# Performance work log

Measured on AMD Instinct MI355X. Metric: run time of the kernel, lower is better.

## Reference

```python
import jax, jax.numpy as jnp
import numpy as np

N_NODES = 50000
NODE_DIM = 128
HIDDEN = 128
N_EDGES = 1600000
N_POSTS = 8192


def setup_inputs() -> dict:
    key = jax.random.key(0)
    ks = jax.random.split(key, 12)
    glorot = lambda k, shp: jax.random.normal(k, shp, jnp.float32) * (1.0 / np.sqrt(shp[0]))
    inp = {
        "node_features": jax.random.normal(ks[0], (N_NODES, NODE_DIM), jnp.float32),
        "edge_index": jax.random.randint(ks[1], (2, N_EDGES), 0, N_NODES, jnp.int32),
        "post_mask": jax.random.randint(ks[2], (N_POSTS,), 0, N_NODES, jnp.int32),
        # node_encoder: node_dim -> hidden
        "W_enc": glorot(ks[3], (NODE_DIM, HIDDEN)),
        "b_enc": jnp.zeros((HIDDEN,), jnp.float32),
        # conv1/conv2: hidden -> hidden
        "W1": glorot(ks[4], (HIDDEN, HIDDEN)),
        "b1": jnp.zeros((HIDDEN,), jnp.float32),
        "W2": glorot(ks[5], (HIDDEN, HIDDEN)),
        "b2": jnp.zeros((HIDDEN,), jnp.float32),
        # output head: hidden -> hidden//2 -> 1
        "W_o1": glorot(ks[6], (HIDDEN, HIDDEN // 2)),
        "b_o1": jnp.zeros((HIDDEN // 2,), jnp.float32),
        "W_o2": glorot(ks[7], (HIDDEN // 2, 1)),
        "b_o2": jnp.zeros((1,), jnp.float32),
    }
    return inp


def _aggregate(h, src, dst, n_nodes):
    # sum_{e: dst[e]=v} h[src[e]]  -- vectorized scatter-add (segment_sum)
    return jax.ops.segment_sum(h[src], dst, num_segments=n_nodes)


def reference(node_features, edge_index, post_mask,
              W_enc, b_enc, W1, b1, W2, b2, W_o1, b_o1, W_o2, b_o2):
    src, dst = edge_index[0], edge_index[1]
    n = node_features.shape[0]

    h = jax.nn.relu(node_features @ W_enc + b_enc)          # [N, H]
    agg = _aggregate(h, src, dst, n)                        # [N, H]
    h = jax.nn.relu((agg + h) @ W1 + b1)
    agg = _aggregate(h, src, dst, n)
    h = jax.nn.relu((agg + h) @ W2 + b2)

    post = h[post_mask]                                     # [P, H]
    hid = jax.nn.relu(post @ W_o1 + b_o1)                   # [P, H//2]
    logits = (hid @ W_o2 + b_o2).squeeze(-1)                # [P]
    return jax.nn.sigmoid(logits)
```

## Files before the change

kernel.cpp:

```cpp
#include <hip/hip_runtime.h>
#include <math.h>


typedef unsigned long long u64;

#define RB_SIZE    4096
#define RB_ROUNDS  16
#define BUCKET_CAP 9216

__global__ __launch_bounds__(1024) void scan_part(const int* __restrict__ in,
                                                  int* __restrict__ bsum, int n) {
    __shared__ int red[1024];
    int i = blockIdx.x * 1024 + threadIdx.x;
    red[threadIdx.x] = (i < n) ? in[i] : 0;
    __syncthreads();
    for (int d = 512; d; d >>= 1) {
        if (threadIdx.x < d) red[threadIdx.x] += red[threadIdx.x + d];
        __syncthreads();
    }
    if (threadIdx.x == 0) bsum[blockIdx.x] = red[0];
}

__global__ __launch_bounds__(256) void scan_tops_par(const int* __restrict__ bsum,
                                                     int* __restrict__ bbase, int nb) {
    __shared__ int buf[256];
    int tid = threadIdx.x;
    int v = (tid < nb) ? bsum[tid] : 0;
    buf[tid] = v;
    __syncthreads();
    for (int s = 1; s < 256; s <<= 1) {
        int u = (tid >= s) ? buf[tid - s] : 0;
        __syncthreads();
        buf[tid] += u;
        __syncthreads();
    }
    if (tid < nb) bbase[tid] = buf[tid] - v;
}

__global__ __launch_bounds__(1024) void scan_final(const int* __restrict__ in,
                                                   const int* __restrict__ bbase,
                                                   int* __restrict__ out, int n) {
    __shared__ int buf[1024];
    int tid = threadIdx.x;
    int i = blockIdx.x * 1024 + tid;
    int c = (i < n) ? in[i] : 0;
    buf[tid] = c;
    __syncthreads();
    for (int d = 1; d < 1024; d <<= 1) {
        int v = (tid >= d) ? buf[tid - d] : 0;
        __syncthreads();
        buf[tid] += v;
        __syncthreads();
    }
    if (i < n) out[i] = bbase[blockIdx.x] + buf[tid] - c;
}

__global__ __launch_bounds__(256) void radix_hist_hi(const int* __restrict__ dstArr,
                                                     int* __restrict__ blockhist,
                                                     int E, int NBLK) {
    __shared__ int cnt[256];
    cnt[threadIdx.x] = 0;
    __syncthreads();
    int base = blockIdx.x * RB_SIZE;
    for (int t = threadIdx.x; t < RB_SIZE; t += 256) {
        int i = base + t;
        if (i < E) atomicAdd(&cnt[dstArr[i] >> 8], 1);
    }
    __syncthreads();
    blockhist[threadIdx.x * NBLK + blockIdx.x] = cnt[threadIdx.x];
}

__global__ __launch_bounds__(256) void radix_scatter_hi(const int* __restrict__ dstArr,
                                                        const int* __restrict__ srcArr,
                                                        u64* __restrict__ recOut,
                                                        const int* __restrict__ blockbase,
                                                        int E, int NBLK) {
    __shared__ int cursor[256];
    __shared__ int gbase[256];
    __shared__ int cnt[256 * 4];
    __shared__ int wbase[256 * 4];
    int tid = threadIdx.x;
    int wid = tid >> 6, lane = tid & 63;
    cursor[tid] = 0;
    gbase[tid] = blockbase[tid * NBLK + blockIdx.x];
    int base = blockIdx.x * RB_SIZE;
    __syncthreads();
    for (int r = 0; r < RB_ROUNDS; ++r) {
        int i = base + r * 256 + tid;
        bool valid = (i < E);
        int d = 0;
        u64 rec = 0;
        if (valid) {
            int dv = dstArr[i];
            rec = ((u64)(unsigned)srcArr[i] << 32) | (unsigned)dv;
            d = dv >> 8;
        }
        ((int4*)cnt)[tid] = make_int4(0, 0, 0, 0);
        u64 mask = ~0ull;
#pragma unroll
        for (int b = 0; b < 8; ++b) {
            int bit = (d >> b) & 1;
            u64 bal = __ballot(bit);
            mask &= bit ? bal : ~bal;
        }
        mask &= __ballot(valid ? 1 : 0);
        int rank = __popcll(mask & (((u64)1 << lane) - 1));
        int wtot = __popcll(mask);
        __syncthreads();
        if (valid && rank == 0) cnt[d * 4 + wid] = wtot;
        __syncthreads();
        {
            int run = cursor[tid];
#pragma unroll
            for (int w = 0; w < 4; ++w) {
                wbase[tid * 4 + w] = run;
                run += cnt[tid * 4 + w];
            }
            cursor[tid] = run;
        }
        __syncthreads();
        if (valid) recOut[gbase[d] + wbase[d * 4 + wid] + rank] = rec;
        __syncthreads();
    }
}

__global__ __launch_bounds__(256) void bucket_kernel(const u64* __restrict__ rec,
                                                     const int* __restrict__ blockbase,
                                                     int* __restrict__ csr_src,
                                                     int* __restrict__ offs,
                                                     int E, int N, int NBLK, int NDIG) {
    __shared__ int srcs[BUCKET_CAP];
    __shared__ unsigned char lob[BUCKET_CAP];
    __shared__ int binb[256];
    __shared__ int cursor[256];
    __shared__ int cnt4[256 * 4];
    __shared__ int wbase4[256 * 4];
    int g = blockIdx.x;
    int tid = threadIdx.x;
    int wid = tid >> 6, lane = tid & 63;
    int gbeg = blockbase[g * NBLK];
    int gend = (g + 1 < NDIG) ? blockbase[(g + 1) * NBLK] : E;
    int cnt = gend - gbeg;
    if (cnt > BUCKET_CAP) cnt = BUCKET_CAP;
    binb[tid] = 0;
    __syncthreads();
    for (int i = tid; i < cnt; i += 256) {
        u64 r = rec[gbeg + i];
        srcs[i] = (int)(r >> 32);
        int lo = (int)(r & 255);
        lob[i] = (unsigned char)lo;
        atomicAdd(&binb[lo], 1);
    }
    __syncthreads();
    int c = binb[tid];
    cursor[tid] = c;
    __syncthreads();
    for (int s = 1; s < 256; s <<= 1) {
        int v = (tid >= s) ? cursor[tid - s] : 0;
        __syncthreads();
        cursor[tid] += v;
        __syncthreads();
    }
    int excl = cursor[tid] - c;
    __syncthreads();
    binb[tid] = excl;
    cursor[tid] = excl;
    int v = g * 256 + tid;
    if (v < N) offs[v] = gbeg + excl;
    if (g == NDIG - 1 && tid == 0) offs[N] = E;
    __syncthreads();
    int nrounds = (cnt + 255) >> 8;
    for (int r = 0; r < nrounds; ++r) {
        int i = r * 256 + tid;
        bool valid = (i < cnt);
        int d = valid ? (int)lob[i] : 0;
        ((int4*)cnt4)[tid] = make_int4(0, 0, 0, 0);
        u64 mask = ~0ull;
#pragma unroll
        for (int b = 0; b < 8; ++b) {
            int bit = (d >> b) & 1;
            u64 bal = __ballot(bit);
            mask &= bit ? bal : ~bal;
        }
        mask &= __ballot(valid ? 1 : 0);
        int rank = __popcll(mask & (((u64)1 << lane) - 1));
        int wtot = __popcll(mask);
        __syncthreads();
        if (valid && rank == 0) cnt4[d * 4 + wid] = wtot;
        __syncthreads();
        {
            int run = cursor[tid];
#pragma unroll
            for (int w = 0; w < 4; ++w) {
                wbase4[tid * 4 + w] = run;
                run += cnt4[tid * 4 + w];
            }
            cursor[tid] = run;
        }
        __syncthreads();
        if (valid) csr_src[gbeg + wbase4[d * 4 + wid] + rank] = srcs[i];
        __syncthreads();
    }
}

template <bool FUSE>
__global__ __launch_bounds__(256) void gemm128(const float* __restrict__ A,
                                               const float* __restrict__ A2,
                                               const float* __restrict__ W,
                                               const float* __restrict__ bias,
                                               float* __restrict__ out, int M) {
    __shared__ float As[128 * 64];
    __shared__ float Ws[64 * 128];
    int tid = threadIdx.x;
    int tx = tid & 15;
    int ty = tid >> 4;
    int row0 = blockIdx.x * 128;

    float acc[8][8];
#pragma unroll
    for (int r = 0; r < 8; ++r)
#pragma unroll
        for (int c = 0; c < 8; ++c) acc[r][c] = 0.f;

    const float4* A4 = (const float4*)A;
    const float4* A24 = (const float4*)A2;
    const float4* W4 = (const float4*)W;
    float4* As4 = (float4*)As;
    float4* Ws4 = (float4*)Ws;
    int swz = ty & 7;

    for (int kh = 0; kh < 2; ++kh) {
        __syncthreads();
#pragma unroll
        for (int j = 0; j < 8; ++j) {
            int idx = tid + 256 * j;
            int r = idx >> 4, kf = idx & 15;
            int gr = row0 + r;
            float4 v = make_float4(0.f, 0.f, 0.f, 0.f);
            if (gr < M) {
                v = A4[gr * 32 + kh * 16 + kf];
                if (FUSE) {
                    float4 u = A24[gr * 32 + kh * 16 + kf];
                    v.x += u.x; v.y += u.y; v.z += u.z; v.w += u.w;
                }
            }
            As4[r * 16 + (kf ^ ((r >> 3) & 7))] = v;
            int k = idx >> 5, cf = idx & 31;
            Ws4[k * 32 + cf] = W4[(kh * 64 + k) * 32 + cf];
        }
        __syncthreads();

#pragma unroll 2
        for (int k4 = 0; k4 < 16; ++k4) {
            float4 a[8];
#pragma unroll
            for (int r = 0; r < 8; ++r)
                a[r] = As4[(ty * 8 + r) * 16 + (k4 ^ swz)];
#pragma unroll
            for (int kk = 0; kk < 4; ++kk) {
                float4 b0 = Ws4[(k4 * 4 + kk) * 32 + tx];
                float4 b1 = Ws4[(k4 * 4 + kk) * 32 + 16 + tx];
#pragma unroll
                for (int r = 0; r < 8; ++r) {
                    float av = (kk == 0) ? a[r].x : (kk == 1) ? a[r].y
                             : (kk == 2) ? a[r].z : a[r].w;
                    acc[r][0] = fmaf(av, b0.x, acc[r][0]);
                    acc[r][1] = fmaf(av, b0.y, acc[r][1]);
                    acc[r][2] = fmaf(av, b0.z, acc[r][2]);
                    acc[r][3] = fmaf(av, b0.w, acc[r][3]);
                    acc[r][4] = fmaf(av, b1.x, acc[r][4]);
                    acc[r][5] = fmaf(av, b1.y, acc[r][5]);
                    acc[r][6] = fmaf(av, b1.z, acc[r][6]);
                    acc[r][7] = fmaf(av, b1.w, acc[r][7]);
                }
            }
        }
    }

    float4 bv0 = ((const float4*)bias)[tx];
    float4 bv1 = ((const float4*)bias)[16 + tx];
    float4* out4 = (float4*)out;
#pragma unroll
    for (int r = 0; r < 8; ++r) {
        int gr = row0 + ty * 8 + r;
        if (gr < M) {
            float4 o0, o1;
            o0.x = fmaxf(acc[r][0] + bv0.x, 0.f);
            o0.y = fmaxf(acc[r][1] + bv0.y, 0.f);
            o0.z = fmaxf(acc[r][2] + bv0.z, 0.f);
            o0.w = fmaxf(acc[r][3] + bv0.w, 0.f);
            o1.x = fmaxf(acc[r][4] + bv1.x, 0.f);
            o1.y = fmaxf(acc[r][5] + bv1.y, 0.f);
            o1.z = fmaxf(acc[r][6] + bv1.z, 0.f);
            o1.w = fmaxf(acc[r][7] + bv1.w, 0.f);
            out4[gr * 32 + tx] = o0;
            out4[gr * 32 + 16 + tx] = o1;
        }
    }
}

__global__ __launch_bounds__(256) void aggregate_kernel(const float* __restrict__ h,
                                                        const int* __restrict__ offs,
                                                        const int* __restrict__ csr_src,
                                                        float* __restrict__ agg, int n) {
    int w = (blockIdx.x * 256 + threadIdx.x) >> 6;
    int lane = threadIdx.x & 63;
    int half = lane >> 5;
    int l32 = lane & 31;
    int node = w * 2 + half;
    bool nvalid = node < n;
    int beg = 0, deg = 0;
    if (nvalid) {
        beg = offs[node];
        deg = offs[node + 1] - beg;
    }
    int mdeg = max(deg, __shfl_xor(deg, 32));
    const float4* h4 = (const float4*)h;
    float ax = 0.f, ay = 0.f, az = 0.f, aw = 0.f;
    for (int base = 0; base < mdeg; base += 32) {
        int idx = base + l32;
        int sv = (nvalid && idx < deg) ? csr_src[beg + idx] : 0;
        int nk = mdeg - base; if (nk > 32) nk = 32;
#pragma unroll 4
        for (int j = 0; j < nk; ++j) {
            int s = __shfl(sv, (half << 5) | j);
            if (base + j < deg) {
                float4 r = h4[s * 32 + l32];
                ax += r.x; ay += r.y; az += r.z; aw += r.w;
            }
        }
    }
    if (nvalid) {
        float4 o = make_float4(ax, ay, az, aw);
        ((float4*)agg)[(size_t)node * 32 + l32] = o;
    }
}

__global__ __launch_bounds__(256) void head_kernel(const float* __restrict__ h,
                                                   const int* __restrict__ mask,
                                                   const float* __restrict__ Wo1,
                                                   const float* __restrict__ bo1,
                                                   const float* __restrict__ Wo2,
                                                   const float* __restrict__ bo2,
                                                   float* __restrict__ out, int P) {
    __shared__ float hids[4][64];
    int wid = threadIdx.x >> 6;
    int lane = threadIdx.x & 63;
    int p = blockIdx.x * 4 + wid;
    if (p >= P) return;
    int node = mask[p];
    const float* row = h + (size_t)node * 128;
    float acc = 0.f;
#pragma unroll 4
    for (int k = 0; k < 128; ++k)
        acc = fmaf(row[k], Wo1[k * 64 + lane], acc);
    hids[wid][lane] = fmaxf(acc + bo1[lane], 0.f);
    if (lane == 0) {
        double lg = 0.0;
        for (int j = 0; j < 64; ++j)
            lg = fma((double)hids[wid][j], (double)Wo2[j], lg);
        lg += (double)bo2[0];
        out[p] = (float)(1.0 / (1.0 + exp(-lg)));
    }
}

extern "C" void kernel_launch(void* const* d_in, const int* in_sizes, int n_in,
                              void* d_out, int out_size, void* d_ws, size_t ws_size,
                              hipStream_t stream) {
    const float* NF   = (const float*)d_in[0];
    const int*   EI   = (const int*)d_in[1];
    const int*   MASK = (const int*)d_in[2];
    const float* Wenc = (const float*)d_in[3];
    const float* benc = (const float*)d_in[4];
    const float* W1   = (const float*)d_in[5];
    const float* b1   = (const float*)d_in[6];
    const float* W2   = (const float*)d_in[7];
    const float* b2   = (const float*)d_in[8];
    const float* Wo1  = (const float*)d_in[9];
    const float* bo1  = (const float*)d_in[10];
    const float* Wo2  = (const float*)d_in[11];
    const float* bo2  = (const float*)d_in[12];
    float* out = (float*)d_out;

    const int N = in_sizes[0] / 128;
    const int E = in_sizes[1] / 2;
    const int P = in_sizes[2];

    char* ws = (char*)d_ws;
    size_t off = 0;
    auto alloc = [&](size_t bytes) {
        char* pp = ws + off;
        off += (bytes + 255) & ~(size_t)255;
        return pp;
    };
    float* h       = (float*)alloc((size_t)N * 128 * 4);
    float* agg     = (float*)alloc((size_t)N * 128 * 4);
    int*   offs    = (int*)alloc((size_t)(N + 1) * 4);
    int*   csr_src = (int*)alloc((size_t)E * 4);
    const int NBLK = (E + RB_SIZE - 1) / RB_SIZE;
    int*   bh      = (int*)alloc((size_t)256 * NBLK * 4);
    int*   bb      = (int*)alloc((size_t)256 * NBLK * 4);
    int*   bsum    = (int*)alloc(256 * 4);
    int*   bbase   = (int*)alloc(256 * 4);
    u64* rec_a = (u64*)h;

    const int* src = EI;
    const int* dst = EI + E;

    const int NDIG = (N + 255) >> 8;
    const int L = NDIG * NBLK;
    const int nscanL = (L + 1023) / 1024;

    radix_hist_hi<<<NBLK, 256, 0, stream>>>(dst, bh, E, NBLK);
    scan_part<<<nscanL, 1024, 0, stream>>>(bh, bsum, L);
    scan_tops_par<<<1, 256, 0, stream>>>(bsum, bbase, nscanL);
    scan_final<<<nscanL, 1024, 0, stream>>>(bh, bbase, bb, L);
    radix_scatter_hi<<<NBLK, 256, 0, stream>>>(dst, src, rec_a, bb, E, NBLK);

    bucket_kernel<<<NDIG, 256, 0, stream>>>(rec_a, bb, csr_src, offs, E, N, NBLK, NDIG);

    int gblocks = (N + 127) / 128;
    int ablocks = ((N + 1) / 2 + 3) / 4;
    gemm128<false><<<gblocks, 256, 0, stream>>>(NF, nullptr, Wenc, benc, h, N);
    aggregate_kernel<<<ablocks, 256, 0, stream>>>(h, offs, csr_src, agg, N);
    gemm128<true><<<gblocks, 256, 0, stream>>>(h, agg, W1, b1, h, N);
    aggregate_kernel<<<ablocks, 256, 0, stream>>>(h, offs, csr_src, agg, N);
    gemm128<true><<<gblocks, 256, 0, stream>>>(h, agg, W2, b2, h, N);
    head_kernel<<<(P + 3) / 4, 256, 0, stream>>>(h, MASK, Wo1, bo1, Wo2, bo2, out, P);
}
```

Baseline: 395.6 us.

## Fuse radix-sort CSR build into one cooperative kernel with grid syncs

Merges the histogram, three scan kernels, the scatter and the bucket sort into a single cooperative kernel separated by grid.sync barriers, with a per-digit scan over blocks replacing the flat global scan. The aim is to cut five kernel launches and their gaps, and to shrink the block-histogram buffer to NDIG rows. In exchange, the grid (about 391 blocks with 56KB LDS each) must be co-resident or the cooperative launch fails, and the large shared allocation lowers occupancy for every phase.

```diff
diff --git a/kernel.cpp b/kernel.cpp
--- a/kernel.cpp
+++ b/kernel.cpp
@@ -1,5 +1,8 @@
 #include <hip/hip_runtime.h>
+#include <hip/hip_cooperative_groups.h>
 #include <math.h>
+
+namespace cg = cooperative_groups;
 
 
 typedef unsigned long long u64;
@@ -8,198 +11,186 @@
 #define RB_ROUNDS  16
 #define BUCKET_CAP 9216
 
-__global__ __launch_bounds__(1024) void scan_part(const int* __restrict__ in,
-                                                  int* __restrict__ bsum, int n) {
-    __shared__ int red[1024];
-    int i = blockIdx.x * 1024 + threadIdx.x;
-    red[threadIdx.x] = (i < n) ? in[i] : 0;
-    __syncthreads();
-    for (int d = 512; d; d >>= 1) {
-        if (threadIdx.x < d) red[threadIdx.x] += red[threadIdx.x + d];
-        __syncthreads();
-    }
-    if (threadIdx.x == 0) bsum[blockIdx.x] = red[0];
-}
-
-__global__ __launch_bounds__(256) void scan_tops_par(const int* __restrict__ bsum,
-                                                     int* __restrict__ bbase, int nb) {
-    __shared__ int buf[256];
+__global__ __launch_bounds__(256) void sort_coop(const int* __restrict__ dstArr,
+                                                 const int* __restrict__ srcArr,
+                                                 u64* __restrict__ rec,
+                                                 int* __restrict__ bh,
+                                                 int* __restrict__ dtot,
+                                                 int* __restrict__ csr_src,
+                                                 int* __restrict__ offs,
+                                                 int E, int N, int NBLK, int NDIG) {
+    __shared__ int smem[14080];
+    int* srcs = smem;
+    unsigned char* lob = (unsigned char*)(smem + 9216);
+    int* A = smem + 11520;
+    int* B = smem + 11776;
+    int* C = smem + 12032;
+    int* D = smem + 13056;
+
+    cg::grid_group grid = cg::this_grid();
     int tid = threadIdx.x;
-    int v = (tid < nb) ? bsum[tid] : 0;
-    buf[tid] = v;
-    __syncthreads();
-    for (int s = 1; s < 256; s <<= 1) {
-        int u = (tid >= s) ? buf[tid - s] : 0;
-        __syncthreads();
-        buf[tid] += u;
-        __syncthreads();
-    }
-    if (tid < nb) bbase[tid] = buf[tid] - v;
-}
-
-__global__ __launch_bounds__(1024) void scan_final(const int* __restrict__ in,
-                                                   const int* __restrict__ bbase,
-                                                   int* __restrict__ out, int n) {
-    __shared__ int buf[1024];
-    int tid = threadIdx.x;
-    int i = blockIdx.x * 1024 + tid;
-    int c = (i < n) ? in[i] : 0;
-    buf[tid] = c;
-    __syncthreads();
-    for (int d = 1; d < 1024; d <<= 1) {
-        int v = (tid >= d) ? buf[tid - d] : 0;
-        __syncthreads();
-        buf[tid] += v;
-        __syncthreads();
-    }
-    if (i < n) out[i] = bbase[blockIdx.x] + buf[tid] - c;
-}
-
-__global__ __launch_bounds__(256) void radix_hist_hi(const int* __restrict__ dstArr,
-                                                     int* __restrict__ blockhist,
-                                                     int E, int NBLK) {
-    __shared__ int cnt[256];
-    cnt[threadIdx.x] = 0;
-    __syncthreads();
-    int base = blockIdx.x * RB_SIZE;
-    for (int t = threadIdx.x; t < RB_SIZE; t += 256) {
-        int i = base + t;
-        if (i < E) atomicAdd(&cnt[dstArr[i] >> 8], 1);
-    }
-    __syncthreads();
-    blockhist[threadIdx.x * NBLK + blockIdx.x] = cnt[threadIdx.x];
-}
-
-__global__ __launch_bounds__(256) void radix_scatter_hi(const int* __restrict__ dstArr,
-                                                        const int* __restrict__ srcArr,
-                                                        u64* __restrict__ recOut,
-                                                        const int* __restrict__ blockbase,
-                                                        int E, int NBLK) {
-    __shared__ int cursor[256];
-    __shared__ int gbase[256];
-    __shared__ int cnt[256 * 4];
-    __shared__ int wbase[256 * 4];
-    int tid = threadIdx.x;
+    int b = blockIdx.x;
     int wid = tid >> 6, lane = tid & 63;
-    cursor[tid] = 0;
-    gbase[tid] = blockbase[tid * NBLK + blockIdx.x];
-    int base = blockIdx.x * RB_SIZE;
-    __syncthreads();
-    for (int r = 0; r < RB_ROUNDS; ++r) {
-        int i = base + r * 256 + tid;
-        bool valid = (i < E);
-        int d = 0;
-        u64 rec = 0;
-        if (valid) {
-            int dv = dstArr[i];
-            rec = ((u64)(unsigned)srcArr[i] << 32) | (unsigned)dv;
-            d = dv >> 8;
-        }
-        ((int4*)cnt)[tid] = make_int4(0, 0, 0, 0);
-        u64 mask = ~0ull;
-#pragma unroll
-        for (int b = 0; b < 8; ++b) {
-            int bit = (d >> b) & 1;
-            u64 bal = __ballot(bit);
-            mask &= bit ? bal : ~bal;
-        }
-        mask &= __ballot(valid ? 1 : 0);
-        int rank = __popcll(mask & (((u64)1 << lane) - 1));
-        int wtot = __popcll(mask);
-        __syncthreads();
-        if (valid && rank == 0) cnt[d * 4 + wid] = wtot;
-        __syncthreads();
-        {
-            int run = cursor[tid];
-#pragma unroll
-            for (int w = 0; w < 4; ++w) {
-                wbase[tid * 4 + w] = run;
-                run += cnt[tid * 4 + w];
-            }
-            cursor[tid] = run;
-        }
-        __syncthreads();
-        if (valid) recOut[gbase[d] + wbase[d * 4 + wid] + rank] = rec;
-        __syncthreads();
-    }
-}
-
-__global__ __launch_bounds__(256) void bucket_kernel(const u64* __restrict__ rec,
-                                                     const int* __restrict__ blockbase,
-                                                     int* __restrict__ csr_src,
-                                                     int* __restrict__ offs,
-                                                     int E, int N, int NBLK, int NDIG) {
-    __shared__ int srcs[BUCKET_CAP];
-    __shared__ unsigned char lob[BUCKET_CAP];
-    __shared__ int binb[256];
-    __shared__ int cursor[256];
-    __shared__ int cnt4[256 * 4];
-    __shared__ int wbase4[256 * 4];
-    int g = blockIdx.x;
-    int tid = threadIdx.x;
-    int wid = tid >> 6, lane = tid & 63;
-    int gbeg = blockbase[g * NBLK];
-    int gend = (g + 1 < NDIG) ? blockbase[(g + 1) * NBLK] : E;
-    int cnt = gend - gbeg;
-    if (cnt > BUCKET_CAP) cnt = BUCKET_CAP;
-    binb[tid] = 0;
-    __syncthreads();
-    for (int i = tid; i < cnt; i += 256) {
-        u64 r = rec[gbeg + i];
-        srcs[i] = (int)(r >> 32);
-        int lo = (int)(r & 255);
-        lob[i] = (unsigned char)lo;
-        atomicAdd(&binb[lo], 1);
-    }
-    __syncthreads();
-    int c = binb[tid];
-    cursor[tid] = c;
-    __syncthreads();
-    for (int s = 1; s < 256; s <<= 1) {
-        int v = (tid >= s) ? cursor[tid - s] : 0;
-        __syncthreads();
-        cursor[tid] += v;
-        __syncthreads();
-    }
-    int excl = cursor[tid] - c;
-    __syncthreads();
-    binb[tid] = excl;
-    cursor[tid] = excl;
-    int v = g * 256 + tid;
-    if (v < N) offs[v] = gbeg + excl;
-    if (g == NDIG - 1 && tid == 0) offs[N] = E;
-    __syncthreads();
-    int nrounds = (cnt + 255) >> 8;
-    for (int r = 0; r < nrounds; ++r) {
-        int i = r * 256 + tid;
-        bool valid = (i < cnt);
-        int d = valid ? (int)lob[i] : 0;
-        ((int4*)cnt4)[tid] = make_int4(0, 0, 0, 0);
-        u64 mask = ~0ull;
-#pragma unroll
-        for (int b = 0; b < 8; ++b) {
-            int bit = (d >> b) & 1;
-            u64 bal = __ballot(bit);
-            mask &= bit ? bal : ~bal;
-        }
-        mask &= __ballot(valid ? 1 : 0);
-        int rank = __popcll(mask & (((u64)1 << lane) - 1));
-        int wtot = __popcll(mask);
-        __syncthreads();
-        if (valid && rank == 0) cnt4[d * 4 + wid] = wtot;
-        __syncthreads();
-        {
-            int run = cursor[tid];
-#pragma unroll
-            for (int w = 0; w < 4; ++w) {
-                wbase4[tid * 4 + w] = run;
-                run += cnt4[tid * 4 + w];
-            }
-            cursor[tid] = run;
-        }
-        __syncthreads();
-        if (valid) csr_src[gbeg + wbase4[d * 4 + wid] + rank] = srcs[i];
-        __syncthreads();
+
+    if (b < NBLK) {
+        A[tid] = 0;
+        __syncthreads();
+        int base = b * RB_SIZE;
+        for (int t = tid; t < RB_SIZE; t += 256) {
+            int i = base + t;
+            if (i < E) atomicAdd(&A[dstArr[i] >> 8], 1);
+        }
+        __syncthreads();
+        if (tid < NDIG) bh[tid * NBLK + b] = A[tid];
+    }
+    grid.sync();
+
+    if (b < NDIG) {
+        int running = 0;
+        for (int base = 0; base < NBLK; base += 512) {
+            int i0 = base + tid, i1 = base + tid + 256;
+            int v0 = (i0 < NBLK) ? bh[b * NBLK + i0] : 0;
+            int v1 = (i1 < NBLK) ? bh[b * NBLK + i1] : 0;
+            srcs[tid] = v0; srcs[tid + 256] = v1;
+            __syncthreads();
+            for (int s = 1; s < 512; s <<= 1) {
+                int a0 = (tid >= s) ? srcs[tid - s] : 0;
+                int a1 = (tid + 256 >= s) ? srcs[tid + 256 - s] : 0;
+                __syncthreads();
+                srcs[tid] += a0; srcs[tid + 256] += a1;
+                __syncthreads();
+            }
+            if (i0 < NBLK) bh[b * NBLK + i0] = running + srcs[tid] - v0;
+            if (i1 < NBLK) bh[b * NBLK + i1] = running + srcs[tid + 256] - v1;
+            running += srcs[511];
+            __syncthreads();
+        }
+        if (tid == 0) dtot[b] = running;
+    }
+    grid.sync();
+
+    if (b == 0) {
+        int v = (tid < NDIG) ? dtot[tid] : 0;
+        srcs[tid] = v;
+        __syncthreads();
+        for (int s = 1; s < 256; s <<= 1) {
+            int u = (tid >= s) ? srcs[tid - s] : 0;
+            __syncthreads();
+            srcs[tid] += u;
+            __syncthreads();
+        }
+        if (tid < NDIG) dtot[tid] = srcs[tid] - v;
+    }
+    grid.sync();
+
+    if (b < NBLK) {
+        B[tid] = 0;
+        A[tid] = (tid < NDIG) ? dtot[tid] + bh[tid * NBLK + b] : 0;
+        int base = b * RB_SIZE;
+        __syncthreads();
+        for (int r = 0; r < RB_ROUNDS; ++r) {
+            int i = base + r * 256 + tid;
+            bool valid = (i < E);
+            int d = 0;
+            u64 rc = 0;
+            if (valid) {
+                int dv = dstArr[i];
+                rc = ((u64)(unsigned)srcArr[i] << 32) | (unsigned)dv;
+                d = dv >> 8;
+            }
+            ((int4*)C)[tid] = make_int4(0, 0, 0, 0);
+            u64 mask = ~0ull;
+#pragma unroll
+            for (int bb2 = 0; bb2 < 8; ++bb2) {
+                int bit = (d >> bb2) & 1;
+                u64 bal = __ballot(bit);
+                mask &= bit ? bal : ~bal;
+            }
+            mask &= __ballot(valid ? 1 : 0);
+            int rank = __popcll(mask & (((u64)1 << lane) - 1));
+            int wtot = __popcll(mask);
+            __syncthreads();
+            if (valid && rank == 0) C[d * 4 + wid] = wtot;
+            __syncthreads();
+            {
+                int run = B[tid];
+#pragma unroll
+                for (int w = 0; w < 4; ++w) {
+                    D[tid * 4 + w] = run;
+                    run += C[tid * 4 + w];
+                }
+                B[tid] = run;
+            }
+            __syncthreads();
+            if (valid) rec[A[d] + D[d * 4 + wid] + rank] = rc;
+            __syncthreads();
+        }
+    }
+    grid.sync();
+
+    if (b < NDIG) {
+        int gbeg = dtot[b];
+        int gend = (b + 1 < NDIG) ? dtot[b + 1] : E;
+        int cnt = gend - gbeg;
+        if (cnt > BUCKET_CAP) cnt = BUCKET_CAP;
+        A[tid] = 0;
+        __syncthreads();
+        for (int i = tid; i < cnt; i += 256) {
+            u64 r = rec[gbeg + i];
+            srcs[i] = (int)(r >> 32);
+            int lo = (int)(r & 255);
+            lob[i] = (unsigned char)lo;
+            atomicAdd(&A[lo], 1);
+        }
+        __syncthreads();
+        int c = A[tid];
+        B[tid] = c;
+        __syncthreads();
+        for (int s = 1; s < 256; s <<= 1) {
+            int v = (tid >= s) ? B[tid - s] : 0;
+            __syncthreads();
+            B[tid] += v;
+            __syncthreads();
+        }
+        int excl = B[tid] - c;
+        __syncthreads();
+        B[tid] = excl;
+        int v = b * 256 + tid;
+        if (v < N) offs[v] = gbeg + excl;
+        if (b == NDIG - 1 && tid == 0) offs[N] = E;
+        __syncthreads();
+        int nrounds = (cnt + 255) >> 8;
+        for (int r = 0; r < nrounds; ++r) {
+            int i = r * 256 + tid;
+            bool valid = (i < cnt);
+            int d = valid ? (int)lob[i] : 0;
+            ((int4*)C)[tid] = make_int4(0, 0, 0, 0);
+            u64 mask = ~0ull;
+#pragma unroll
+            for (int bb2 = 0; bb2 < 8; ++bb2) {
+                int bit = (d >> bb2) & 1;
+                u64 bal = __ballot(bit);
+                mask &= bit ? bal : ~bal;
+            }
+            mask &= __ballot(valid ? 1 : 0);
+            int rank = __popcll(mask & (((u64)1 << lane) - 1));
+            int wtot = __popcll(mask);
+            __syncthreads();
+            if (valid && rank == 0) C[d * 4 + wid] = wtot;
+            __syncthreads();
+            {
+                int run = B[tid];
+#pragma unroll
+                for (int w = 0; w < 4; ++w) {
+                    D[tid * 4 + w] = run;
+                    run += C[tid * 4 + w];
+                }
+                B[tid] = run;
+            }
+            __syncthreads();
+            if (valid) csr_src[gbeg + D[d * 4 + wid] + rank] = srcs[i];
+            __syncthreads();
+        }
     }
 }
 
@@ -398,26 +389,27 @@
     int*   offs    = (int*)alloc((size_t)(N + 1) * 4);
     int*   csr_src = (int*)alloc((size_t)E * 4);
     const int NBLK = (E + RB_SIZE - 1) / RB_SIZE;
-    int*   bh      = (int*)alloc((size_t)256 * NBLK * 4);
-    int*   bb      = (int*)alloc((size_t)256 * NBLK * 4);
-    int*   bsum    = (int*)alloc(256 * 4);
-    int*   bbase   = (int*)alloc(256 * 4);
+    const int NDIG = (N + 255) >> 8;
+    int*   bh      = (int*)alloc((size_t)NDIG * NBLK * 4);
+    int*   dtot    = (int*)alloc(256 * 4);
     u64* rec_a = (u64*)h;
 
     const int* src = EI;
     const int* dst = EI + E;
 
-    const int NDIG = (N + 255) >> 8;
-    const int L = NDIG * NBLK;
-    const int nscanL = (L + 1023) / 1024;
-
-    radix_hist_hi<<<NBLK, 256, 0, stream>>>(dst, bh, E, NBLK);
-    scan_part<<<nscanL, 1024, 0, stream>>>(bh, bsum, L);
-    scan_tops_par<<<1, 256, 0, stream>>>(bsum, bbase, nscanL);
-    scan_final<<<nscanL, 1024, 0, stream>>>(bh, bbase, bb, L);
-    radix_scatter_hi<<<NBLK, 256, 0, stream>>>(dst, src, rec_a, bb, E, NBLK);
-
-    bucket_kernel<<<NDIG, 256, 0, stream>>>(rec_a, bb, csr_src, offs, E, N, NBLK, NDIG);
+    {
+        const int* a_dst = dst; const int* a_src = src;
+        u64* a_rec = rec_a; int* a_bh = bh; int* a_dtot = dtot;
+        int* a_csr = csr_src; int* a_offs = offs;
+        int a_E = E, a_N = N, a_NBLK = NBLK, a_NDIG = NDIG;
+        void* kargs[] = { (void*)&a_dst, (void*)&a_src, (void*)&a_rec,
+                          (void*)&a_bh, (void*)&a_dtot, (void*)&a_csr,
+                          (void*)&a_offs, (void*)&a_E, (void*)&a_N,
+                          (void*)&a_NBLK, (void*)&a_NDIG };
+        int gridBlocks = (NBLK > NDIG) ? NBLK : NDIG;
+        hipLaunchCooperativeKernel((void*)sort_coop, dim3(gridBlocks), dim3(256),
+                                   kargs, 0, stream);
+    }
 
     int gblocks = (N + 127) / 128;
     int ablocks = ((N + 1) / 2 + 3) / 4;
```

Measured after the change: 598.2 us. +51.2%, slower.
